# Kernel optimization log

Measured on AMD Instinct MI355X. Metric: run time of the kernel, lower is better.

The kernel has to match this reference:

```python
import jax, jax.numpy as jnp
import numpy as np

CUTOFF = 5.0
P = 6               # envelope polynomial power
NUM_RBF = 6
NUM_SBF = 7
EMBED = 128
TYPE_EMBED = 64
OUT_EMBED = 256
INT_EMBED = 64      # angle_int_embed_size
BASIS_EMBED = 8
N_BLOCKS = 4
N_DENSE_OUT = 3
N_RES_BEFORE = 1
N_RES_AFTER = 2
N_SPECIES = 16
NUM_TARGETS = 1
N_ATOMS = 4096
N_EDGES = 65536
N_TRIPLETS = 524288

# first 6 positive roots of spherical Bessel j_l, l = 0..6
BESSEL_ZEROS = np.array([
    [3.141593, 6.283185, 9.424778, 12.566371, 15.707963, 18.849556],
    [4.493409, 7.725252, 10.904122, 14.066194, 17.220755, 20.371303],
    [5.763459, 9.095011, 12.322941, 15.514603, 18.689036, 21.853874],
    [6.987932, 10.417119, 13.698023, 16.923621, 20.121806, 23.304247],
    [8.182561, 11.704907, 15.039665, 18.301256, 21.525418, 24.727566],
    [9.355812, 12.966530, 16.354710, 19.653152, 22.904551, 26.126750],
    [10.512835, 14.207392, 17.647975, 20.983463, 24.262768, 27.507868]], dtype=np.float32)

act = jax.nn.silu  # swish


def envelope(x):
    a = -(P + 1) * (P + 2) / 2.0
    b = float(P * (P + 2))
    c = -P * (P + 1) / 2.0
    env = 1.0 / x + a * x ** (P - 1) + b * x ** P + c * x ** (P + 1)
    return jnp.where(x < 1.0, env, 0.0)


def radial_bessel(d):
    # d: (E,) -> (E, NUM_RBF)
    x = d / CUTOFF
    n = jnp.arange(1, NUM_RBF + 1, dtype=jnp.float32)
    return np.float32(np.sqrt(2.0 / CUTOFF)) * envelope(x)[:, None] * jnp.sin(jnp.pi * n[None, :] * x[:, None])


def spherical_basis(d_kj, angles, triplet_mask):
    # d_kj: (T,), angles: (T,) -> (T, NUM_SBF * NUM_RBF)
    x = jnp.maximum(d_kj / CUTOFF, 1e-6)
    env = envelope(x)
    zeros = jnp.asarray(BESSEL_ZEROS)
    radial = []
    for l in range(NUM_SBF):
        a = zeros[l][None, :] * x[:, None]           # (T, NUM_RBF)
        j0 = jnp.sin(a) / a
        if l == 0:
            radial.append(j0)
            continue
        j1 = jnp.sin(a) / a ** 2 - jnp.cos(a) / a
        jm2, jm1 = j0, j1
        for ll in range(2, l + 1):
            jm2, jm1 = jm1, (2 * ll - 1) / a * jm1 - jm2
        radial.append(jm1)
    radial = jnp.stack(radial, axis=1)               # (T, NUM_SBF, NUM_RBF)
    ct = jnp.cos(angles)
    Pl = [jnp.ones_like(ct), ct]
    for l in range(2, NUM_SBF):
        Pl.append(((2 * l - 1) * ct * Pl[l - 1] - (l - 1) * Pl[l - 2]) / l)
    sph = jnp.stack([np.float32(np.sqrt((2 * l + 1) / (4.0 * np.pi))) * Pl[l] for l in range(NUM_SBF)], axis=1)  # (T, NUM_SBF)
    sbf = (env[:, None, None] * radial * sph[:, :, None]).reshape(-1, NUM_SBF * NUM_RBF)
    return jnp.where(triplet_mask[:, None], sbf, 0.0)


def _forward(distances, angles, species_embed, emb_rbf_w, emb_rbf_b, emb_dense_w, emb_dense_b,
             out_rbf_w, out_up_w, out_dense_w, out_dense_b, out_final_w,
             int_ji_w, int_ji_b, int_kj_w, int_kj_b, int_rbf1_w, int_rbf2_w, int_down_w,
             int_sbf1_w, int_sbf2_w, int_up_w, int_res1_w, int_res1_b, int_skip_w, int_skip_b,
             int_res2_w, int_res2_b,
             species, idx_i, idx_j, reduce_to_ji, expand_to_kj, edge_mask, triplet_mask):
    n_particles = species.shape[0]
    n_edges = distances.shape[0]
    d = jnp.where(edge_mask, distances, 2.0 * CUTOFF)       # masked edges -> env = 0
    rbf = radial_bessel(d)                                  # (E, 6)
    sbf = spherical_basis(d[expand_to_kj], angles, triplet_mask)  # (T, 42)

    # embedding block
    h = species_embed[species]                              # (N, 64)
    rbf_emb = rbf @ emb_rbf_w + emb_rbf_b                   # (E, 128)
    m = act(jnp.concatenate([h[idx_j], h[idx_i], rbf_emb], axis=-1) @ emb_dense_w + emb_dense_b)

    def output_block(i, msg):
        atom = jax.ops.segment_sum((rbf @ out_rbf_w[i]) * msg, idx_i, num_segments=n_particles)
        atom = atom @ out_up_w[i]
        for k in range(N_DENSE_OUT):
            atom = act(atom @ out_dense_w[i, k] + out_dense_b[i, k])
        return atom @ out_final_w[i]

    out = output_block(0, m)
    for i in range(N_BLOCKS):
        x_ji = act(m @ int_ji_w[i] + int_ji_b[i])
        x_kj = act(m @ int_kj_w[i] + int_kj_b[i])
        x_kj = x_kj * ((rbf @ int_rbf1_w[i]) @ int_rbf2_w[i])
        x_kj = act(x_kj @ int_down_w[i])                    # (E, 64)
        x_kj = x_kj[expand_to_kj] * ((sbf @ int_sbf1_w[i]) @ int_sbf2_w[i])  # (T, 64)
        x_kj = jax.ops.segment_sum(x_kj, reduce_to_ji, num_segments=n_edges)
        x_kj = act(x_kj @ int_up_w[i])
        hm = x_ji + x_kj
        for r in range(N_RES_BEFORE):
            hm = hm + act(act(hm @ int_res1_w[i, r, 0] + int_res1_b[i, r, 0]) @ int_res1_w[i, r, 1] + int_res1_b[i, r, 1])
        m = act(hm @ int_skip_w[i] + int_skip_b[i]) + m
        for r in range(N_RES_AFTER):
            m = m + act(act(m @ int_res2_w[i, r, 0] + int_res2_b[i, r, 0]) @ int_res2_w[i, r, 1] + int_res2_b[i, r, 1])
        out = out + output_block(i + 1, m)
    return out


def setup_inputs() -> dict:
    key = jax.random.key(0)
    ks = iter(jax.random.split(key, 40))
    def nrm(shape, fan_in):
        return jax.random.normal(next(ks), shape, dtype=jnp.float32) / np.float32(np.sqrt(fan_in))
    inp = {}
    inp['distances'] = 0.5 + 4.45 * jax.random.uniform(next(ks), (N_EDGES,), dtype=jnp.float32)
    inp['angles'] = jnp.pi * jax.random.uniform(next(ks), (N_TRIPLETS,), dtype=jnp.float32)
    inp['species_embed'] = jax.random.normal(next(ks), (N_SPECIES, TYPE_EMBED), dtype=jnp.float32)
    inp['emb_rbf_w'] = nrm((NUM_RBF, EMBED), NUM_RBF)
    inp['emb_rbf_b'] = jnp.zeros((EMBED,), jnp.float32)
    inp['emb_dense_w'] = nrm((2 * TYPE_EMBED + EMBED, EMBED), 2 * TYPE_EMBED + EMBED)
    inp['emb_dense_b'] = jnp.zeros((EMBED,), jnp.float32)
    nb1 = N_BLOCKS + 1
    inp['out_rbf_w'] = nrm((nb1, NUM_RBF, EMBED), NUM_RBF)
    inp['out_up_w'] = nrm((nb1, EMBED, OUT_EMBED), EMBED)
    inp['out_dense_w'] = nrm((nb1, N_DENSE_OUT, OUT_EMBED, OUT_EMBED), OUT_EMBED)
    inp['out_dense_b'] = jnp.zeros((nb1, N_DENSE_OUT, OUT_EMBED), jnp.float32)
    inp['out_final_w'] = nrm((nb1, OUT_EMBED, NUM_TARGETS), OUT_EMBED)
    inp['int_ji_w'] = nrm((N_BLOCKS, EMBED, EMBED), EMBED)
    inp['int_ji_b'] = jnp.zeros((N_BLOCKS, EMBED), jnp.float32)
    inp['int_kj_w'] = nrm((N_BLOCKS, EMBED, EMBED), EMBED)
    inp['int_kj_b'] = jnp.zeros((N_BLOCKS, EMBED), jnp.float32)
    inp['int_rbf1_w'] = nrm((N_BLOCKS, NUM_RBF, BASIS_EMBED), NUM_RBF)
    inp['int_rbf2_w'] = nrm((N_BLOCKS, BASIS_EMBED, EMBED), BASIS_EMBED)
    inp['int_down_w'] = nrm((N_BLOCKS, EMBED, INT_EMBED), EMBED)
    inp['int_sbf1_w'] = nrm((N_BLOCKS, NUM_SBF * NUM_RBF, BASIS_EMBED), NUM_SBF * NUM_RBF)
    inp['int_sbf2_w'] = nrm((N_BLOCKS, BASIS_EMBED, INT_EMBED), BASIS_EMBED)
    inp['int_up_w'] = nrm((N_BLOCKS, INT_EMBED, EMBED), INT_EMBED)
    inp['int_res1_w'] = nrm((N_BLOCKS, N_RES_BEFORE, 2, EMBED, EMBED), EMBED)
    inp['int_res1_b'] = jnp.zeros((N_BLOCKS, N_RES_BEFORE, 2, EMBED), jnp.float32)
    inp['int_skip_w'] = nrm((N_BLOCKS, EMBED, EMBED), EMBED)
    inp['int_skip_b'] = jnp.zeros((N_BLOCKS, EMBED), jnp.float32)
    inp['int_res2_w'] = nrm((N_BLOCKS, N_RES_AFTER, 2, EMBED, EMBED), EMBED)
    inp['int_res2_b'] = jnp.zeros((N_BLOCKS, N_RES_AFTER, 2, EMBED), jnp.float32)
    inp['species'] = jax.random.randint(next(ks), (N_ATOMS,), 0, N_SPECIES)
    inp['idx_i'] = jax.random.randint(next(ks), (N_EDGES,), 0, N_ATOMS)
    inp['idx_j'] = jax.random.randint(next(ks), (N_EDGES,), 0, N_ATOMS)
    inp['reduce_to_ji'] = jax.random.randint(next(ks), (N_TRIPLETS,), 0, N_EDGES)
    inp['expand_to_kj'] = jax.random.randint(next(ks), (N_TRIPLETS,), 0, N_EDGES)
    inp['edge_mask'] = jnp.ones((N_EDGES,), dtype=bool)
    inp['triplet_mask'] = jnp.ones((N_TRIPLETS,), dtype=bool)
    return inp


def reference(distances, angles, species_embed, emb_rbf_w, emb_rbf_b, emb_dense_w, emb_dense_b,
              out_rbf_w, out_up_w, out_dense_w, out_dense_b, out_final_w,
              int_ji_w, int_ji_b, int_kj_w, int_kj_b, int_rbf1_w, int_rbf2_w, int_down_w,
              int_sbf1_w, int_sbf2_w, int_up_w, int_res1_w, int_res1_b, int_skip_w, int_skip_b,
              int_res2_w, int_res2_b,
              species, idx_i, idx_j, reduce_to_ji, expand_to_kj, edge_mask, triplet_mask):
    return _forward(distances, angles, species_embed, emb_rbf_w, emb_rbf_b, emb_dense_w, emb_dense_b,
                    out_rbf_w, out_up_w, out_dense_w, out_dense_b, out_final_w,
                    int_ji_w, int_ji_b, int_kj_w, int_kj_b, int_rbf1_w, int_rbf2_w, int_down_w,
                    int_sbf1_w, int_sbf2_w, int_up_w, int_res1_w, int_res1_b, int_skip_w, int_skip_b,
                    int_res2_w, int_res2_b,
                    species, idx_i, idx_j, reduce_to_ji, expand_to_kj, edge_mask, triplet_mask)
```

## Files before the change

### kernel.cpp

```cpp
#include <hip/hip_runtime.h>
#include <cmath>

typedef __attribute__((ext_vector_type(8))) short bfrag;
typedef __attribute__((ext_vector_type(4))) float f32x4;

__device__ __forceinline__ float silu_f(float x) {
    return x * __builtin_amdgcn_rcpf(1.0f + __expf(-x));
}
__device__ __forceinline__ unsigned short f2bf(float f) {
    unsigned u = __float_as_uint(f);
    unsigned r = (u + 0x7fff + ((u >> 16) & 1)) >> 16;
    return (unsigned short)r;
}
__device__ __forceinline__ float bf2f(unsigned short h) {
    return __uint_as_float(((unsigned)h) << 16);
}
__device__ __forceinline__ unsigned packbf2(float lo, float hi) {
    return ((unsigned)f2bf(hi) << 16) | (unsigned)f2bf(lo);
}
__device__ __forceinline__ unsigned cvtpk2(float a, float b) {
    unsigned r;
    asm("v_cvt_pk_bf16_f32 %0, %1, %2" : "=v"(r) : "v"(a), "v"(b));
    return r;
}
__device__ __forceinline__ uint2 pk4(float a, float b, float c, float d) {
    return make_uint2(cvtpk2(a, b), cvtpk2(c, d));
}

template <int KSTEPS, int S, int NS, int ST>
__device__ __forceinline__ void mfma_stage_T(
    const unsigned short* Xs,
    const unsigned short* __restrict__ Whi, const unsigned short* __restrict__ Wlo,
    int Kdim, int arow0, int bcol0, int r16, int kg, f32x4 (&acc)[S][NS]) {
    #pragma unroll
    for (int s = 0; s < S; s++)
        #pragma unroll
        for (int ns = 0; ns < NS; ns++) acc[s][ns] = (f32x4)0.f;
    #pragma unroll
    for (int ks = 0; ks < KSTEPS; ks++) {
        int k0 = ks * 32;
        bfrag wh[NS], wl[NS];
        #pragma unroll
        for (int ns = 0; ns < NS; ns++) {
            size_t o = (size_t)(bcol0 + ns * 16 + r16) * Kdim + k0 + kg * 8;
            wh[ns] = *(const bfrag*)&Whi[o];
            wl[ns] = *(const bfrag*)&Wlo[o];
        }
        #pragma unroll
        for (int s = 0; s < S; s++) {
            bfrag xh = *(const bfrag*)&Xs[(arow0 + s * 16 + r16) * ST + k0 + kg * 8];
            #pragma unroll
            for (int ns = 0; ns < NS; ns++) {
                acc[s][ns] = __builtin_amdgcn_mfma_f32_16x16x32_bf16(wh[ns], xh, acc[s][ns], 0, 0, 0);
                acc[s][ns] = __builtin_amdgcn_mfma_f32_16x16x32_bf16(wl[ns], xh, acc[s][ns], 0, 0, 0);
            }
        }
    }
}

__global__ __launch_bounds__(256) void rbf_kernel(const float* __restrict__ d,
                                                  float* __restrict__ rbf, int E) {
    int e = blockIdx.x * 256 + threadIdx.x;
    if (e >= E) return;
    float x = d[e] * 0.2f;
    float env = 0.0f;
    if (x < 1.0f) {
        float x2 = x * x;
        float x5 = x2 * x2 * x;
        env = 1.0f / x + x5 * (-28.0f + x * (48.0f - 21.0f * x));
    }
    const float SQ = 0.63245553f;
    float px = 3.14159265358979f * x;
    #pragma unroll
    for (int n = 1; n <= 6; n++) {
        rbf[e * 6 + n - 1] = SQ * env * __sinf(px * (float)n);
    }
}

__global__ __launch_bounds__(128) void embed_pre_kernel(
    const float* __restrict__ se, const float* __restrict__ erw,
    const float* __restrict__ erb, const float* __restrict__ edw,
    float* __restrict__ HWj, float* __restrict__ HWi,
    float* __restrict__ W3, float* __restrict__ b3) {
    int c = threadIdx.x;
    for (int s = 0; s < 16; s++) {
        float aj = 0.f, ai = 0.f;
        for (int k = 0; k < 64; k++) {
            float h = se[s * 64 + k];
            aj += h * edw[k * 128 + c];
            ai += h * edw[(64 + k) * 128 + c];
        }
        HWj[s * 128 + c] = aj;
        HWi[s * 128 + c] = ai;
    }
    for (int r = 0; r < 6; r++) {
        float a = 0.f;
        for (int k = 0; k < 128; k++) a += erw[r * 128 + k] * edw[(128 + k) * 128 + c];
        W3[r * 128 + c] = a;
    }
    float a = 0.f;
    for (int k = 0; k < 128; k++) a += erb[k] * edw[(128 + k) * 128 + c];
    b3[c] = a;
}

__global__ __launch_bounds__(256) void embed_kernel(
    const float* __restrict__ rbf, const int* __restrict__ species,
    const int* __restrict__ idx_i, const int* __restrict__ idx_j,
    const float* __restrict__ HWj, const float* __restrict__ HWi,
    const float* __restrict__ W3, const float* __restrict__ b3,
    const float* __restrict__ edb, float* __restrict__ m) {
    int gid = blockIdx.x * 256 + threadIdx.x;
    int e = gid >> 7, c = gid & 127;
    int sj = species[idx_j[e]];
    int si = species[idx_i[e]];
    float v = HWj[sj * 128 + c] + HWi[si * 128 + c] + b3[c] + edb[c];
    #pragma unroll
    for (int k = 0; k < 6; k++) v += rbf[e * 6 + k] * W3[k * 128 + c];
    m[gid] = silu_f(v);
}

__global__ __launch_bounds__(256) void wconv_kernel(
    const float* __restrict__ W, unsigned short* __restrict__ hi,
    unsigned short* __restrict__ lo, int K, int N) {
    __shared__ float t[32][33];
    int b = blockIdx.z;
    int n0 = blockIdx.x * 32, k0 = blockIdx.y * 32;
    const float* Wb = W + (size_t)b * K * N;
    int tid = threadIdx.x;
    int r = tid >> 3, cg = tid & 7;
    float4 v = *(const float4*)&Wb[(size_t)(k0 + r) * N + n0 + cg * 4];
    t[r][cg * 4 + 0] = v.x;
    t[r][cg * 4 + 1] = v.y;
    t[r][cg * 4 + 2] = v.z;
    t[r][cg * 4 + 3] = v.w;
    __syncthreads();
    int nl = tid >> 3, kg = tid & 7;
    short4 h4, l4;
// ... 39 lines not shown
        bfrag wh[2], wl[2];
        #pragma unroll
        for (int ns = 0; ns < 2; ns++) {
            size_t o = (size_t)(bn + bcol0 + ns * 16 + r16) * K + k0 + kg * 8;
            wh[ns] = *(const bfrag*)&Whi[o];
            wl[ns] = *(const bfrag*)&Wlo[o];
        }
        #pragma unroll
        for (int s = 0; s < 2; s++) {
            bfrag xh = *(const bfrag*)&Xs[(arow0 + s * 16 + r16) * 40 + kg * 8];
            #pragma unroll
            for (int ns = 0; ns < 2; ns++) {
                acc[s][ns] = __builtin_amdgcn_mfma_f32_16x16x32_bf16(wh[ns], xh, acc[s][ns], 0, 0, 0);
                acc[s][ns] = __builtin_amdgcn_mfma_f32_16x16x32_bf16(wl[ns], xh, acc[s][ns], 0, 0, 0);
            }
        }
        __syncthreads();
    }
    #pragma unroll
    for (int s = 0; s < 2; s++) {
        int mm = bm + arow0 + s * 16 + r16;
        #pragma unroll
        for (int ns = 0; ns < 2; ns++) {
            int n0 = bn + bcol0 + ns * 16 + kg * 4;
            float bv[4] = {0.f, 0.f, 0.f, 0.f};
            if (BIAS) {
                float4 b4 = *(const float4*)&bias[n0];
                bv[0] = b4.x; bv[1] = b4.y; bv[2] = b4.z; bv[3] = b4.w;
            }
            float4 o;
            float* op = (float*)&o;
            #pragma unroll
            for (int r = 0; r < 4; r++) {
                float v = acc[s][ns][r] + bv[r];
                if (ACT) v = silu_f(v);
                op[r] = v;
            }
            if (RES) {
                float4 rv = *(const float4*)&resid[(size_t)mm * N + n0];
                o.x += rv.x; o.y += rv.y; o.z += rv.z; o.w += rv.w;
            }
            *(float4*)&Y[(size_t)mm * N + n0] = o;
        }
    }
}

__global__ __launch_bounds__(512, 4) void outchain_kernel(
    const float* __restrict__ atom2,
    const unsigned short* __restrict__ odh, const unsigned short* __restrict__ odl,
    const float* __restrict__ odb, const float* __restrict__ wf,
    float* __restrict__ out) {
    __shared__ unsigned short Xs[64 * 264];
    __shared__ float rsum[64];
    int tid = threadIdx.x, bm = blockIdx.x * 64;
    int wid = tid >> 6, lane = tid & 63;
    int wr = wid >> 2, wc = wid & 3;
    int r16 = lane & 15, kg = lane >> 4;
    int arow0 = wr * 32, bcol0 = wc * 64;
    if (tid < 64) rsum[tid] = 0.f;

    #pragma unroll
    for (int p = 0; p < 8; p++) {
        int idx = tid + p * 512, row = idx >> 6, cg = idx & 63;
        float4 v = *(const float4*)&atom2[(size_t)(bm + row) * 256 + cg * 4];
        *(uint2*)&Xs[row * 264 + cg * 4] = pk4(v.x, v.y, v.z, v.w);
    }
    __syncthreads();

    f32x4 acc[2][4];
    #pragma unroll
    for (int st = 0; st < 3; st++) {
        mfma_stage_T<8, 2, 4, 264>(Xs, odh + (size_t)st * 65536, odl + (size_t)st * 65536,
                                   256, arow0, bcol0, r16, kg, acc);
        const float* bb = odb + st * 256;
        __syncthreads();
        if (st < 2) {
            #pragma unroll
            for (int s = 0; s < 2; s++)
                #pragma unroll
                for (int ns = 0; ns < 4; ns++) {
                    int n0 = bcol0 + ns * 16 + kg * 4;
                    float4 b4 = *(const float4*)&bb[n0];
                    *(uint2*)&Xs[(arow0 + s * 16 + r16) * 264 + n0] =
                        pk4(silu_f(acc[s][0 + ns][0] + b4.x), silu_f(acc[s][ns][1] + b4.y),
                            silu_f(acc[s][ns][2] + b4.z), silu_f(acc[s][ns][3] + b4.w));
                }
            __syncthreads();
        } else {
            #pragma unroll
            for (int s = 0; s < 2; s++) {
                float part = 0.f;
                #pragma unroll
                for (int ns = 0; ns < 4; ns++) {
                    int n0 = bcol0 + ns * 16 + kg * 4;
                    float4 b4 = *(const float4*)&bb[n0];
                    float4 w4 = *(const float4*)&wf[n0];
                    part += silu_f(acc[s][ns][0] + b4.x) * w4.x;
                    part += silu_f(acc[s][ns][1] + b4.y) * w4.y;
                    part += silu_f(acc[s][ns][2] + b4.z) * w4.z;
                    part += silu_f(acc[s][ns][3] + b4.w) * w4.w;
                }
                atomicAdd(&rsum[arow0 + s * 16 + r16], part);
            }
        }
    }
    __syncthreads();
    if (tid < 64) out[bm + tid] += rsum[tid];
}

__global__ __launch_bounds__(512, 4) void downpath_kernel(
    const float* __restrict__ m, const float* __restrict__ rbf,
    const float* __restrict__ rbf1, const float* __restrict__ rbf2,
    const unsigned short* __restrict__ jih, const unsigned short* __restrict__ jil,
    const float* __restrict__ jib,
    const unsigned short* __restrict__ kjh, const unsigned short* __restrict__ kjl,
    const float* __restrict__ kjb,
    const unsigned short* __restrict__ dnh, const unsigned short* __restrict__ dnl,
    float* __restrict__ xji, float* __restrict__ xdown) {
    __shared__ unsigned short Xs[64 * 136];
    __shared__ float G8t[8][64];
    __shared__ float Rs[8][128];
    int tid = threadIdx.x, bm = blockIdx.x * 64;
    int wid = tid >> 6, lane = tid & 63;
    int wr = wid >> 2, wc = wid & 3;
    int r16 = lane & 15, kg = lane >> 4;
    int arow0 = wr * 32, bcol0 = wc * 32;

    #pragma unroll
    for (int p = 0; p < 4; p++) {
        int idx = tid + p * 512, row = idx >> 5, cg = idx & 31;
        float4 v = *(const float4*)&m[(size_t)(bm + row) * 128 + cg * 4];
        *(uint2*)&Xs[row * 136 + cg * 4] = pk4(v.x, v.y, v.z, v.w);
    }
    if (tid < 64) {
        float rv[6];
        #pragma unroll
        for (int k = 0; k < 6; k++) rv[k] = rbf[(size_t)(bm + tid) * 6 + k];
        #pragma unroll
        for (int p = 0; p < 8; p++) {
            float a = 0.f;
            #pragma unroll
            for (int k = 0; k < 6; k++) a += rv[k] * rbf1[k * 8 + p];
            G8t[p][tid] = a;
        }
    }
    for (int i = tid; i < 1024; i += 512) Rs[i >> 7][i & 127] = rbf2[i];
    __syncthreads();

    f32x4 acc[2][2];
    mfma_stage_T<4, 2, 2, 136>(Xs, jih, jil, 128, arow0, bcol0, r16, kg, acc);
    #pragma unroll
    for (int s = 0; s < 2; s++) {
        int mm = bm + arow0 + s * 16 + r16;
        #pragma unroll
        for (int ns = 0; ns < 2; ns++) {
            int n0 = bcol0 + ns * 16 + kg * 4;
            float4 b4 = *(const float4*)&jib[n0];
            float4 o;
            o.x = silu_f(acc[s][ns][0] + b4.x);
            o.y = silu_f(acc[s][ns][1] + b4.y);
            o.z = silu_f(acc[s][ns][2] + b4.z);
            o.w = silu_f(acc[s][ns][3] + b4.w);
            *(float4*)&xji[(size_t)mm * 128 + n0] = o;
        }
    }
    mfma_stage_T<4, 2, 2, 136>(Xs, kjh, kjl, 128, arow0, bcol0, r16, kg, acc);
    f32x4 val[2][2];
    #pragma unroll
    for (int s = 0; s < 2; s++) {
        int mrow = arow0 + s * 16 + r16;
        float g8v[8];
        #pragma unroll
        for (int p = 0; p < 8; p++) g8v[p] = G8t[p][mrow];
        #pragma unroll
        for (int ns = 0; ns < 2; ns++) {
            int n0 = bcol0 + ns * 16 + kg * 4;
            float4 b4 = *(const float4*)&kjb[n0];
            float bb[4] = {b4.x, b4.y, b4.z, b4.w};
            #pragma unroll
            for (int r = 0; r < 4; r++) {
                float g = 0.f;
                #pragma unroll
                for (int p = 0; p < 8; p++) g = fmaf(g8v[p], Rs[p][n0 + r], g);
                val[s][ns][r] = silu_f(acc[s][ns][r] + bb[r]) * g;
            }
        }
    }
    __syncthreads();
    #pragma unroll
    for (int s = 0; s < 2; s++)
        #pragma unroll
        for (int ns = 0; ns < 2; ns++)
            *(uint2*)&Xs[(arow0 + s * 16 + r16) * 136 + bcol0 + ns * 16 + kg * 4] =
                pk4(val[s][ns][0], val[s][ns][1], val[s][ns][2], val[s][ns][3]);
    __syncthreads();
    {
        int ar2 = (wid >> 1) * 16, wc2 = wid & 1;
        f32x4 a2[1][2];
        mfma_stage_T<4, 1, 2, 136>(Xs, dnh, dnl, 128, ar2, wc2 * 32, r16, kg, a2);
        int mm = bm + ar2 + r16;
        #pragma unroll
        for (int ns = 0; ns < 2; ns++) {
            int n0 = wc2 * 32 + ns * 16 + kg * 4;
            float4 o;
            o.x = silu_f(a2[0][ns][0]);
            o.y = silu_f(a2[0][ns][1]);
            o.z = silu_f(a2[0][ns][2]);
            o.w = silu_f(a2[0][ns][3]);
            *(float4*)&xdown[(size_t)mm * 64 + n0] = o;
        }
    }
}

__global__ __launch_bounds__(512, 4) void chain_kernel(
    const float* __restrict__ seg, const float* __restrict__ xji, float* __restrict__ m,
    const unsigned short* __restrict__ uph, const unsigned short* __restrict__ upl,
    const unsigned short* __restrict__ r1h, const unsigned short* __restrict__ r1l,
    const float* __restrict__ r1b,
    const unsigned short* __restrict__ skh, const unsigned short* __restrict__ skl,
    const float* __restrict__ skb,
    const unsigned short* __restrict__ r2h, const unsigned short* __restrict__ r2l,
    const float* __restrict__ r2b) {
    __shared__ unsigned short Xs[64 * 136];
    int tid = threadIdx.x, bm = blockIdx.x * 64;
    int wid = tid >> 6, lane = tid & 63;
    int wr = wid >> 2, wc = wid & 3;
    int r16 = lane & 15, kg = lane >> 4;
    int arow0 = wr * 32, bcol0 = wc * 32;

    #pragma unroll
    for (int p = 0; p < 2; p++) {
        int idx = tid + p * 512, row = idx >> 4, cg = idx & 15;
        float4 v = *(const float4*)&seg[(size_t)(bm + row) * 64 + cg * 4];
        *(uint2*)&Xs[row * 136 + cg * 4] = pk4(v.x, v.y, v.z, v.w);
    }
    __syncthreads();

    f32x4 acc[2][2], res[2][2];

    mfma_stage_T<2, 2, 2, 136>(Xs, uph, upl, 64, arow0, bcol0, r16, kg, acc);
    #pragma unroll
    for (int s = 0; s < 2; s++) {
        int mm = bm + arow0 + s * 16 + r16;
        #pragma unroll
        for (int ns = 0; ns < 2; ns++) {
            int n0 = bcol0 + ns * 16 + kg * 4;
            float4 xv = *(const float4*)&xji[(size_t)mm * 128 + n0];
            res[s][ns][0] = silu_f(acc[s][ns][0]) + xv.x;
            res[s][ns][1] = silu_f(acc[s][ns][1]) + xv.y;
            res[s][ns][2] = silu_f(acc[s][ns][2]) + xv.z;
            res[s][ns][3] = silu_f(acc[s][ns][3]) + xv.w;
        }
    }
    __syncthreads();
    #pragma unroll
    for (int s = 0; s < 2; s++)
        #pragma unroll
        for (int ns = 0; ns < 2; ns++)
            *(uint2*)&Xs[(arow0 + s * 16 + r16) * 136 + bcol0 + ns * 16 + kg * 4] =
                pk4(res[s][ns][0], res[s][ns][1], res[s][ns][2], res[s][ns][3]);
    __syncthreads();

    mfma_stage_T<4, 2, 2, 136>(Xs, r1h, r1l, 128, arow0, bcol0, r16, kg, acc);
    __syncthreads();
    #pragma unroll
    for (int s = 0; s < 2; s++)
        #pragma unroll
        for (int ns = 0; ns < 2; ns++) {
            int n0 = bcol0 + ns * 16 + kg * 4;
            float4 b4 = *(const float4*)&r1b[n0];
            *(uint2*)&Xs[(arow0 + s * 16 + r16) * 136 + n0] =
                pk4(silu_f(acc[s][ns][0] + b4.x), silu_f(acc[s][ns][1] + b4.y),
                    silu_f(acc[s][ns][2] + b4.z), silu_f(acc[s][ns][3] + b4.w));
        }
    __syncthreads();
    mfma_stage_T<4, 2, 2, 136>(Xs, r1h + 16384, r1l + 16384, 128, arow0, bcol0, r16, kg, acc);
    #pragma unroll
    for (int s = 0; s < 2; s++)
        #pragma unroll
        for (int ns = 0; ns < 2; ns++) {
            int n0 = bcol0 + ns * 16 + kg * 4;
            float4 b4 = *(const float4*)&r1b[128 + n0];
            res[s][ns][0] += silu_f(acc[s][ns][0] + b4.x);
            res[s][ns][1] += silu_f(acc[s][ns][1] + b4.y);
            res[s][ns][2] += silu_f(acc[s][ns][2] + b4.z);
            res[s][ns][3] += silu_f(acc[s][ns][3] + b4.w);
        }
    __syncthreads();
    #pragma unroll
    for (int s = 0; s < 2; s++)
        #pragma unroll
        for (int ns = 0; ns < 2; ns++)
            *(uint2*)&Xs[(arow0 + s * 16 + r16) * 136 + bcol0 + ns * 16 + kg * 4] =
                pk4(res[s][ns][0], res[s][ns][1], res[s][ns][2], res[s][ns][3]);
    __syncthreads();

    mfma_stage_T<4, 2, 2, 136>(Xs, skh, skl, 128, arow0, bcol0, r16, kg, acc);
    #pragma unroll
    for (int s = 0; s < 2; s++) {
        int mm = bm + arow0 + s * 16 + r16;
        #pragma unroll
        for (int ns = 0; ns < 2; ns++) {
            int n0 = bcol0 + ns * 16 + kg * 4;
            float4 b4 = *(const float4*)&skb[n0];
            float4 mv = *(const float4*)&m[(size_t)mm * 128 + n0];
            res[s][ns][0] = silu_f(acc[s][ns][0] + b4.x) + mv.x;
            res[s][ns][1] = silu_f(acc[s][ns][1] + b4.y) + mv.y;
            res[s][ns][2] = silu_f(acc[s][ns][2] + b4.z) + mv.z;
            res[s][ns][3] = silu_f(acc[s][ns][3] + b4.w) + mv.w;
        }
    }
    __syncthreads();
    #pragma unroll
    for (int s = 0; s < 2; s++)
        #pragma unroll
        for (int ns = 0; ns < 2; ns++)
            *(uint2*)&Xs[(arow0 + s * 16 + r16) * 136 + bcol0 + ns * 16 + kg * 4] =
                pk4(res[s][ns][0], res[s][ns][1], res[s][ns][2], res[s][ns][3]);
    __syncthreads();

    #pragma unroll
    for (int rr = 0; rr < 2; rr++) {
        const unsigned short* wh = r2h + (size_t)rr * 2 * 16384;
        const unsigned short* wl = r2l + (size_t)rr * 2 * 16384;
        const float* bb = r2b + (size_t)rr * 2 * 128;
        mfma_stage_T<4, 2, 2, 136>(Xs, wh, wl, 128, arow0, bcol0, r16, kg, acc);
        __syncthreads();
        #pragma unroll
        for (int s = 0; s < 2; s++)
            #pragma unroll
            for (int ns = 0; ns < 2; ns++) {
                int n0 = bcol0 + ns * 16 + kg * 4;
                float4 b4 = *(const float4*)&bb[n0];
                *(uint2*)&Xs[(arow0 + s * 16 + r16) * 136 + n0] =
                    pk4(silu_f(acc[s][ns][0] + b4.x), silu_f(acc[s][ns][1] + b4.y),
                        silu_f(acc[s][ns][2] + b4.z), silu_f(acc[s][ns][3] + b4.w));
            }
        __syncthreads();
        mfma_stage_T<4, 2, 2, 136>(Xs, wh + 16384, wl + 16384, 128, arow0, bcol0, r16, kg, acc);
        #pragma unroll
        for (int s = 0; s < 2; s++)
            #pragma unroll
            for (int ns = 0; ns < 2; ns++) {
                int n0 = bcol0 + ns * 16 + kg * 4;
                float4 b4 = *(const float4*)&bb[128 + n0];
                res[s][ns][0] += silu_f(acc[s][ns][0] + b4.x);
                res[s][ns][1] += silu_f(acc[s][ns][1] + b4.y);
                res[s][ns][2] += silu_f(acc[s][ns][2] + b4.z);
                res[s][ns][3] += silu_f(acc[s][ns][3] + b4.w);
            }
        if (rr == 0) {
            __syncthreads();
            #pragma unroll
            for (int s = 0; s < 2; s++)
                #pragma unroll
                for (int ns = 0; ns < 2; ns++)
                    *(uint2*)&Xs[(arow0 + s * 16 + r16) * 136 + bcol0 + ns * 16 + kg * 4] =
                        pk4(res[s][ns][0], res[s][ns][1], res[s][ns][2], res[s][ns][3]);
            __syncthreads();
        }
    }
    #pragma unroll
    for (int s = 0; s < 2; s++) {
        int mm = bm + arow0 + s * 16 + r16;
        #pragma unroll
        for (int ns = 0; ns < 2; ns++) {
            int n0 = bcol0 + ns * 16 + kg * 4;
            float4 o;
            o.x = res[s][ns][0]; o.y = res[s][ns][1];
            o.z = res[s][ns][2]; o.w = res[s][ns][3];
            *(float4*)&m[(size_t)mm * 128 + n0] = o;
        }
    }
}

__global__ __launch_bounds__(256) void outseg_kernel(
    const float* __restrict__ rbf, const float* __restrict__ orw,
    const float* __restrict__ m, const int* __restrict__ idx_i,
    float* __restrict__ atom) {
    int gid = blockIdx.x * 256 + threadIdx.x;
    int e = gid >> 7, c = gid & 127;
    float s = 0.f;
    #pragma unroll
    for (int k = 0; k < 6; k++) s += rbf[e * 6 + k] * orw[k * 128 + c];
    atomicAdd(&atom[(size_t)idx_i[e] * 128 + c], s * m[gid]);
}

__global__ __launch_bounds__(256) void hist_kernel(const int* __restrict__ rji,
                                                   int* __restrict__ hist) {
    int t = blockIdx.x * 256 + threadIdx.x;
    atomicAdd(&hist[rji[t]], 1);
}

__global__ __launch_bounds__(256) void scan1_kernel(const int* __restrict__ hist,
                                                    int* __restrict__ bsum) {
    __shared__ int s[256];
    int i = threadIdx.x;
    s[i] = hist[blockIdx.x * 256 + i];
    __syncthreads();
    for (int o = 128; o; o >>= 1) {
        if (i < o) s[i] += s[i + o];
        __syncthreads();
    }
    if (!i) bsum[blockIdx.x] = s[0];
}

__global__ __launch_bounds__(256) void scan2_kernel(const int* __restrict__ bsum,
                                                    int* __restrict__ boff) {
    __shared__ int s[256];
    int i = threadIdx.x;
    int own = bsum[i];
    s[i] = own;
    __syncthreads();
    for (int o = 1; o < 256; o <<= 1) {
        int v = (i >= o) ? s[i - o] : 0;
        __syncthreads();
        s[i] += v;
        __syncthreads();
    }
    boff[i] = s[i] - own;
}

__global__ __launch_bounds__(256) void scan3_kernel(const int* __restrict__ hist,
                                                    const int* __restrict__ boff,
                                                    int* __restrict__ rows,
                                                    int* __restrict__ cursor, int T) {
    __shared__ int s[256];
    int i = threadIdx.x, b = blockIdx.x;
    int h = hist[b * 256 + i];
    s[i] = h;
    __syncthreads();
    for (int o = 1; o < 256; o <<= 1) {
        int v = (i >= o) ? s[i - o] : 0;
        __syncthreads();
        s[i] += v;
        __syncthreads();
    }
    int excl = s[i] - h + boff[b];
    rows[b * 256 + i] = excl;
    cursor[b * 256 + i] = excl;
    if (b == gridDim.x - 1 && i == 255) rows[b * 256 + 256] = T;
}

__global__ __launch_bounds__(256) void scatter_kernel(
    const int* __restrict__ rji, const int* __restrict__ ekj,
    int* __restrict__ cursor, int* __restrict__ perm, int* __restrict__ ekjs) {
// ... 165 lines not shown
    float* HWj = ws + off;   off += 16 * 128;
    float* HWi = ws + off;   off += 16 * 128;
    float* W3  = ws + off;   off += 6 * 128;
    float* b3  = ws + off;   off += 128;
    float* atom1 = ws + off; off += (size_t)NA * 128;
    float* atom2 = ws + off; off += (size_t)NA * 256;
    float* atom3 = ws + off; off += (size_t)NA * 256;
    float* seg = B;

    unsigned short* wb = (unsigned short*)(ws + off);
    size_t wo = 0;
    unsigned short* ji_h = wb + wo;  wo += 4 * 16384;
    unsigned short* ji_l = wb + wo;  wo += 4 * 16384;
    unsigned short* kj_h = wb + wo;  wo += 4 * 16384;
    unsigned short* kj_l = wb + wo;  wo += 4 * 16384;
    unsigned short* dn_h = wb + wo;  wo += 4 * 8192;
    unsigned short* dn_l = wb + wo;  wo += 4 * 8192;
    unsigned short* up_h = wb + wo;  wo += 4 * 8192;
    unsigned short* up_l = wb + wo;  wo += 4 * 8192;
    unsigned short* r1_h = wb + wo;  wo += 8 * 16384;
    unsigned short* r1_l = wb + wo;  wo += 8 * 16384;
    unsigned short* sk_h = wb + wo;  wo += 4 * 16384;
    unsigned short* sk_l = wb + wo;  wo += 4 * 16384;
    unsigned short* r2_h = wb + wo;  wo += 16 * 16384;
    unsigned short* r2_l = wb + wo;  wo += 16 * 16384;
    unsigned short* ou_h = wb + wo;  wo += 5 * 32768;
    unsigned short* ou_l = wb + wo;  wo += 5 * 32768;
    unsigned short* od_h = wb + wo;  wo += 15 * 65536;
    unsigned short* od_l = wb + wo;  wo += 15 * 65536;
    unsigned short* t32 = wb + wo;   wo += (size_t)4 * T * 8;
    int* ip    = (int*)(wb + wo);
    size_t io  = 0;
    int* hist   = ip + io;  io += E;
    int* rows   = ip + io;  io += E + 64;
    int* cursor = ip + io;  io += E;
    int* bsum   = ip + io;  io += 256;
    int* boff   = ip + io;  io += 256;
    int* perm   = ip + io;  io += T;
    int* ekjs   = ip + io;  io += T;

    float* out = (float*)d_out;
    hipMemsetAsync(out, 0, (size_t)out_size * sizeof(float), stream);

    hipMemsetAsync(hist, 0, (size_t)E * sizeof(int), stream);
    hist_kernel<<<T / 256, 256, 0, stream>>>(reduce_ji, hist);
    scan1_kernel<<<E / 256, 256, 0, stream>>>(hist, bsum);
    scan2_kernel<<<1, 256, 0, stream>>>(bsum, boff);
    scan3_kernel<<<E / 256, 256, 0, stream>>>(hist, boff, rows, cursor, T);
    scatter_kernel<<<T / 256, 256, 0, stream>>>(reduce_ji, expand_kj, cursor, perm, ekjs);
    sbf_pre_kernel<<<T / 256, 256, 0, stream>>>(distances, angles, perm, ekjs,
                                                int_sbf1_w, t32, T);

    wconv_kernel<<<dim3(4, 4, 4), 256, 0, stream>>>(int_ji_w, ji_h, ji_l, 128, 128);
    wconv_kernel<<<dim3(4, 4, 4), 256, 0, stream>>>(int_kj_w, kj_h, kj_l, 128, 128);
    wconv_kernel<<<dim3(2, 4, 4), 256, 0, stream>>>(int_down_w, dn_h, dn_l, 128, 64);
    wconv_kernel<<<dim3(4, 2, 4), 256, 0, stream>>>(int_up_w, up_h, up_l, 64, 128);
    wconv_kernel<<<dim3(4, 4, 8), 256, 0, stream>>>(int_res1_w, r1_h, r1_l, 128, 128);
    wconv_kernel<<<dim3(4, 4, 4), 256, 0, stream>>>(int_skip_w, sk_h, sk_l, 128, 128);
    wconv_kernel<<<dim3(4, 4, 16), 256, 0, stream>>>(int_res2_w, r2_h, r2_l, 128, 128);
    wconv_kernel<<<dim3(8, 4, 5), 256, 0, stream>>>(out_up_w, ou_h, ou_l, 128, 256);
    wconv_kernel<<<dim3(8, 8, 15), 256, 0, stream>>>(out_dense_w, od_h, od_l, 256, 256);

    rbf_kernel<<<E / 256, 256, 0, stream>>>(distances, rbf, E);
    embed_pre_kernel<<<1, 128, 0, stream>>>(species_emb, emb_rbf_w, emb_rbf_b,
                                            emb_dense_w, HWj, HWi, W3, b3);
    embed_kernel<<<E * 128 / 256, 256, 0, stream>>>(rbf, species, idx_i, idx_j,
                                                    HWj, HWi, W3, b3, emb_dense_b, m);

    auto outblock = [&](int i, const float* msg) {
        hipMemsetAsync(atom1, 0, (size_t)NA * 128 * sizeof(float), stream);
        outseg_kernel<<<E * 128 / 256, 256, 0, stream>>>(
            rbf, out_rbf_w + (size_t)i * 6 * 128, msg, idx_i, atom1);
        mfma_gemmT<0, 0, 0><<<dim3(NA / 64, 2), 512, 0, stream>>>(
            atom1, ou_h + (size_t)i * 32768, ou_l + (size_t)i * 32768,
            nullptr, nullptr, atom2, NA, 128, 256);
        outchain_kernel<<<NA / 64, 512, 0, stream>>>(
            atom2, od_h + (size_t)i * 3 * 65536, od_l + (size_t)i * 3 * 65536,
            out_dense_b + (size_t)i * 3 * 256, out_final_w + (size_t)i * 256, out);
    };

    outblock(0, m);

    for (int i = 0; i < 4; i++) {
        downpath_kernel<<<E / 64, 512, 0, stream>>>(
            m, rbf, int_rbf1_w + (size_t)i * 48, int_rbf2_w + (size_t)i * 1024,
            ji_h + (size_t)i * 16384, ji_l + (size_t)i * 16384, int_ji_b + (size_t)i * 128,
            kj_h + (size_t)i * 16384, kj_l + (size_t)i * 16384, int_kj_b + (size_t)i * 128,
            dn_h + (size_t)i * 8192, dn_l + (size_t)i * 8192,
            A, D);
        seg_gather_kernel<<<E * 64 / 256, 256, 0, stream>>>(
            t32 + (size_t)i * T * 8, ekjs, rows, D,
            int_sbf2_w + (size_t)i * 8 * 64, seg, E);
        chain_kernel<<<E / 64, 512, 0, stream>>>(
            seg, A, m,
            up_h + (size_t)i * 8192, up_l + (size_t)i * 8192,
            r1_h + (size_t)i * 32768, r1_l + (size_t)i * 32768, int_res1_b + (size_t)i * 256,
            sk_h + (size_t)i * 16384, sk_l + (size_t)i * 16384, int_skip_b + (size_t)i * 128,
            r2_h + (size_t)i * 65536, r2_l + (size_t)i * 65536, int_res2_b + (size_t)i * 512);
        outblock(i + 1, m);
    }
}
```

Baseline: 1.742 ms.

## Enlarge row tiles, double-buffer LDS and prefetch weights in chain kernels

Doubles the row tile of the downpath and chain kernels from 64 to 128 edges, so each warp computes four 16-row subtiles and every loaded weight fragment is reused across more rows. Adds ping-pong LDS buffers (XsA/XsB), which removes the barrier that had to come before each activation write-back. Adds a new MFMA stage that prefetches the next K-step of weights into registers. In exchange the kernels use more registers and about 70KB of LDS per block, which lowers occupancy and halves the grid size.

```diff
diff --git a/kernel.cpp b/kernel.cpp
--- a/kernel.cpp
+++ b/kernel.cpp
@@ -53,6 +53,45 @@
             for (int ns = 0; ns < NS; ns++) {
                 acc[s][ns] = __builtin_amdgcn_mfma_f32_16x16x32_bf16(wh[ns], xh, acc[s][ns], 0, 0, 0);
                 acc[s][ns] = __builtin_amdgcn_mfma_f32_16x16x32_bf16(wl[ns], xh, acc[s][ns], 0, 0, 0);
+            }
+        }
+    }
+}
+
+template <int KSTEPS, int S, int NS, int ST>
+__device__ __forceinline__ void mfma_stage_pp(
+    const unsigned short* Xs,
+    const unsigned short* __restrict__ Whi, const unsigned short* __restrict__ Wlo,
+    int Kdim, int arow0, int bcol0, int r16, int kg, f32x4 (&acc)[S][NS]) {
+    bfrag wh[2][NS], wl[2][NS];
+    #pragma unroll
+    for (int ns = 0; ns < NS; ns++) {
+        size_t o = (size_t)(bcol0 + ns * 16 + r16) * Kdim + kg * 8;
+        wh[0][ns] = *(const bfrag*)&Whi[o];
+        wl[0][ns] = *(const bfrag*)&Wlo[o];
+    }
+    #pragma unroll
+    for (int s = 0; s < S; s++)
+        #pragma unroll
+        for (int ns = 0; ns < NS; ns++) acc[s][ns] = (f32x4)0.f;
+    #pragma unroll
+    for (int ks = 0; ks < KSTEPS; ks++) {
+        const int cur = ks & 1, nxt = cur ^ 1;
+        if (ks + 1 < KSTEPS) {
+            #pragma unroll
+            for (int ns = 0; ns < NS; ns++) {
+                size_t o = (size_t)(bcol0 + ns * 16 + r16) * Kdim + (ks + 1) * 32 + kg * 8;
+                wh[nxt][ns] = *(const bfrag*)&Whi[o];
+                wl[nxt][ns] = *(const bfrag*)&Wlo[o];
+            }
+        }
+        #pragma unroll
+        for (int s = 0; s < S; s++) {
+            bfrag xh = *(const bfrag*)&Xs[(arow0 + s * 16 + r16) * ST + ks * 32 + kg * 8];
+            #pragma unroll
+            for (int ns = 0; ns < NS; ns++) {
+                acc[s][ns] = __builtin_amdgcn_mfma_f32_16x16x32_bf16(wh[cur][ns], xh, acc[s][ns], 0, 0, 0);
+                acc[s][ns] = __builtin_amdgcn_mfma_f32_16x16x32_bf16(wl[cur][ns], xh, acc[s][ns], 0, 0, 0);
             }
         }
     }
@@ -258,7 +297,7 @@
                     int n0 = bcol0 + ns * 16 + kg * 4;
                     float4 b4 = *(const float4*)&bb[n0];
                     *(uint2*)&Xs[(arow0 + s * 16 + r16) * 264 + n0] =
-                        pk4(silu_f(acc[s][0 + ns][0] + b4.x), silu_f(acc[s][ns][1] + b4.y),
+                        pk4(silu_f(acc[s][ns][0] + b4.x), silu_f(acc[s][ns][1] + b4.y),
                             silu_f(acc[s][ns][2] + b4.z), silu_f(acc[s][ns][3] + b4.w));
                 }
             __syncthreads();
@@ -293,22 +332,23 @@
     const float* __restrict__ kjb,
     const unsigned short* __restrict__ dnh, const unsigned short* __restrict__ dnl,
     float* __restrict__ xji, float* __restrict__ xdown) {
-    __shared__ unsigned short Xs[64 * 136];
-    __shared__ float G8t[8][64];
+    __shared__ unsigned short XsA[128 * 136];
+    __shared__ unsigned short XsB[128 * 136];
+    __shared__ float G8t[8][128];
     __shared__ float Rs[8][128];
-    int tid = threadIdx.x, bm = blockIdx.x * 64;
+    int tid = threadIdx.x, bm = blockIdx.x * 128;
     int wid = tid >> 6, lane = tid & 63;
     int wr = wid >> 2, wc = wid & 3;
     int r16 = lane & 15, kg = lane >> 4;
-    int arow0 = wr * 32, bcol0 = wc * 32;
-
-    #pragma unroll
-    for (int p = 0; p < 4; p++) {
+    int arow0 = wr * 64, bcol0 = wc * 32;
+
+    #pragma unroll
+    for (int p = 0; p < 8; p++) {
         int idx = tid + p * 512, row = idx >> 5, cg = idx & 31;
         float4 v = *(const float4*)&m[(size_t)(bm + row) * 128 + cg * 4];
-        *(uint2*)&Xs[row * 136 + cg * 4] = pk4(v.x, v.y, v.z, v.w);
-    }
-    if (tid < 64) {
+        *(uint2*)&XsA[row * 136 + cg * 4] = pk4(v.x, v.y, v.z, v.w);
+    }
+    if (tid < 128) {
         float rv[6];
         #pragma unroll
         for (int k = 0; k < 6; k++) rv[k] = rbf[(size_t)(bm + tid) * 6 + k];
@@ -323,10 +363,10 @@
     for (int i = tid; i < 1024; i += 512) Rs[i >> 7][i & 127] = rbf2[i];
     __syncthreads();
 
-    f32x4 acc[2][2];
-    mfma_stage_T<4, 2, 2, 136>(Xs, jih, jil, 128, arow0, bcol0, r16, kg, acc);
-    #pragma unroll
-    for (int s = 0; s < 2; s++) {
+    f32x4 acc[4][2];
+    mfma_stage_pp<4, 4, 2, 136>(XsA, jih, jil, 128, arow0, bcol0, r16, kg, acc);
+    #pragma unroll
+    for (int s = 0; s < 4; s++) {
         int mm = bm + arow0 + s * 16 + r16;
         #pragma unroll
         for (int ns = 0; ns < 2; ns++) {
@@ -340,10 +380,9 @@
             *(float4*)&xji[(size_t)mm * 128 + n0] = o;
         }
     }
-    mfma_stage_T<4, 2, 2, 136>(Xs, kjh, kjl, 128, arow0, bcol0, r16, kg, acc);
-    f32x4 val[2][2];
-    #pragma unroll
-    for (int s = 0; s < 2; s++) {
+    mfma_stage_pp<4, 4, 2, 136>(XsA, kjh, kjl, 128, arow0, bcol0, r16, kg, acc);
+    #pragma unroll
+    for (int s = 0; s < 4; s++) {
         int mrow = arow0 + s * 16 + r16;
         float g8v[8];
         #pragma unroll
@@ -353,37 +392,36 @@
             int n0 = bcol0 + ns * 16 + kg * 4;
             float4 b4 = *(const float4*)&kjb[n0];
             float bb[4] = {b4.x, b4.y, b4.z, b4.w};
+            float v[4];
             #pragma unroll
             for (int r = 0; r < 4; r++) {
                 float g = 0.f;
                 #pragma unroll
                 for (int p = 0; p < 8; p++) g = fmaf(g8v[p], Rs[p][n0 + r], g);
-                val[s][ns][r] = silu_f(acc[s][ns][r] + bb[r]) * g;
-            }
-        }
-    }
-    __syncthreads();
-    #pragma unroll
-    for (int s = 0; s < 2; s++)
-        #pragma unroll
-        for (int ns = 0; ns < 2; ns++)
-            *(uint2*)&Xs[(arow0 + s * 16 + r16) * 136 + bcol0 + ns * 16 + kg * 4] =
-                pk4(val[s][ns][0], val[s][ns][1], val[s][ns][2], val[s][ns][3]);
+                v[r] = silu_f(acc[s][ns][r] + bb[r]) * g;
+            }
+            *(uint2*)&XsB[mrow * 136 + n0] = pk4(v[0], v[1], v[2], v[3]);
+        }
+    }
     __syncthreads();
     {
-        int ar2 = (wid >> 1) * 16, wc2 = wid & 1;
-        f32x4 a2[1][2];
-        mfma_stage_T<4, 1, 2, 136>(Xs, dnh, dnl, 128, ar2, wc2 * 32, r16, kg, a2);
-        int mm = bm + ar2 + r16;
-        #pragma unroll
-        for (int ns = 0; ns < 2; ns++) {
-            int n0 = wc2 * 32 + ns * 16 + kg * 4;
-            float4 o;
-            o.x = silu_f(a2[0][ns][0]);
-            o.y = silu_f(a2[0][ns][1]);
-            o.z = silu_f(a2[0][ns][2]);
-            o.w = silu_f(a2[0][ns][3]);
-            *(float4*)&xdown[(size_t)mm * 64 + n0] = o;
+        int wr2 = wid >> 1, wc2 = wid & 1;
+        int ar2 = wr2 * 32, bc2 = wc2 * 32;
+        f32x4 a2[2][2];
+        mfma_stage_pp<4, 2, 2, 136>(XsB, dnh, dnl, 128, ar2, bc2, r16, kg, a2);
+        #pragma unroll
+        for (int s = 0; s < 2; s++) {
+            int mm = bm + ar2 + s * 16 + r16;
+            #pragma unroll
+            for (int ns = 0; ns < 2; ns++) {
+                int n0 = bc2 + ns * 16 + kg * 4;
+                float4 o;
+                o.x = silu_f(a2[s][ns][0]);
+                o.y = silu_f(a2[s][ns][1]);
+                o.z = silu_f(a2[s][ns][2]);
+                o.w = silu_f(a2[s][ns][3]);
+                *(float4*)&xdown[(size_t)mm * 64 + n0] = o;
+            }
         }
     }
 }
@@ -397,26 +435,61 @@
     const float* __restrict__ skb,
     const unsigned short* __restrict__ r2h, const unsigned short* __restrict__ r2l,
     const float* __restrict__ r2b) {
-    __shared__ unsigned short Xs[64 * 136];
-    int tid = threadIdx.x, bm = blockIdx.x * 64;
+    __shared__ unsigned short XsA[128 * 136];
+    __shared__ unsigned short XsB[128 * 136];
+    int tid = threadIdx.x, bm = blockIdx.x * 128;
     int wid = tid >> 6, lane = tid & 63;
     int wr = wid >> 2, wc = wid & 3;
     int r16 = lane & 15, kg = lane >> 4;
-    int arow0 = wr * 32, bcol0 = wc * 32;
-
-    #pragma unroll
-    for (int p = 0; p < 2; p++) {
+    int arow0 = wr * 64, bcol0 = wc * 32;
+
+    #pragma unroll
+    for (int p = 0; p < 4; p++) {
         int idx = tid + p * 512, row = idx >> 4, cg = idx & 15;
         float4 v = *(const float4*)&seg[(size_t)(bm + row) * 64 + cg * 4];
-        *(uint2*)&Xs[row * 136 + cg * 4] = pk4(v.x, v.y, v.z, v.w);
-    }
-    __syncthreads();
-
-    f32x4 acc[2][2], res[2][2];
-
-    mfma_stage_T<2, 2, 2, 136>(Xs, uph, upl, 64, arow0, bcol0, r16, kg, acc);
-    #pragma unroll
-    for (int s = 0; s < 2; s++) {
+        *(uint2*)&XsA[row * 136 + cg * 4] = pk4(v.x, v.y, v.z, v.w);
+    }
+    __syncthreads();
+
+    f32x4 acc[4][2], res[4][2];
+
+    auto store_frags = [&](unsigned short* Xd, const f32x4 (&v)[4][2]) {
+        #pragma unroll
+        for (int s = 0; s < 4; s++)
+            #pragma unroll
+            for (int ns = 0; ns < 2; ns++)
+                *(uint2*)&Xd[(arow0 + s * 16 + r16) * 136 + bcol0 + ns * 16 + kg * 4] =
+                    pk4(v[s][ns][0], v[s][ns][1], v[s][ns][2], v[s][ns][3]);
+    };
+    auto store_act = [&](unsigned short* Xd, const f32x4 (&a)[4][2], const float* bb) {
+        #pragma unroll
+        for (int s = 0; s < 4; s++)
+            #pragma unroll
+            for (int ns = 0; ns < 2; ns++) {
+                int n0 = bcol0 + ns * 16 + kg * 4;
+                float4 b4 = *(const float4*)&bb[n0];
+                *(uint2*)&Xd[(arow0 + s * 16 + r16) * 136 + n0] =
+                    pk4(silu_f(a[s][ns][0] + b4.x), silu_f(a[s][ns][1] + b4.y),
+                        silu_f(a[s][ns][2] + b4.z), silu_f(a[s][ns][3] + b4.w));
+            }
+    };
+    auto accum_res = [&](const f32x4 (&a)[4][2], const float* bb) {
+        #pragma unroll
+        for (int s = 0; s < 4; s++)
+            #pragma unroll
+            for (int ns = 0; ns < 2; ns++) {
+                int n0 = bcol0 + ns * 16 + kg * 4;
+                float4 b4 = *(const float4*)&bb[n0];
+                res[s][ns][0] += silu_f(a[s][ns][0] + b4.x);
+                res[s][ns][1] += silu_f(a[s][ns][1] + b4.y);
+                res[s][ns][2] += silu_f(a[s][ns][2] + b4.z);
+                res[s][ns][3] += silu_f(a[s][ns][3] + b4.w);
+            }
+    };
+
+    mfma_stage_pp<2, 4, 2, 136>(XsA, uph, upl, 64, arow0, bcol0, r16, kg, acc);
+    #pragma unroll
+    for (int s = 0; s < 4; s++) {
         int mm = bm + arow0 + s * 16 + r16;
         #pragma unroll
         for (int ns = 0; ns < 2; ns++) {
@@ -428,52 +501,20 @@
             res[s][ns][3] = silu_f(acc[s][ns][3]) + xv.w;
         }
     }
-    __syncthreads();
-    #pragma unroll
-    for (int s = 0; s < 2; s++)
-        #pragma unroll
-        for (int ns = 0; ns < 2; ns++)
-            *(uint2*)&Xs[(arow0 + s * 16 + r16) * 136 + bcol0 + ns * 16 + kg * 4] =
-                pk4(res[s][ns][0], res[s][ns][1], res[s][ns][2], res[s][ns][3]);
-    __syncthreads();
-
-    mfma_stage_T<4, 2, 2, 136>(Xs, r1h, r1l, 128, arow0, bcol0, r16, kg, acc);
-    __syncthreads();
-    #pragma unroll
-    for (int s = 0; s < 2; s++)
-        #pragma unroll
-        for (int ns = 0; ns < 2; ns++) {
-            int n0 = bcol0 + ns * 16 + kg * 4;
-            float4 b4 = *(const float4*)&r1b[n0];
-            *(uint2*)&Xs[(arow0 + s * 16 + r16) * 136 + n0] =
-                pk4(silu_f(acc[s][ns][0] + b4.x), silu_f(acc[s][ns][1] + b4.y),
-                    silu_f(acc[s][ns][2] + b4.z), silu_f(acc[s][ns][3] + b4.w));
-        }
-    __syncthreads();
-    mfma_stage_T<4, 2, 2, 136>(Xs, r1h + 16384, r1l + 16384, 128, arow0, bcol0, r16, kg, acc);
-    #pragma unroll
-    for (int s = 0; s < 2; s++)
-        #pragma unroll
-        for (int ns = 0; ns < 2; ns++) {
-            int n0 = bcol0 + ns * 16 + kg * 4;
-            float4 b4 = *(const float4*)&r1b[128 + n0];
-            res[s][ns][0] += silu_f(acc[s][ns][0] + b4.x);
-            res[s][ns][1] += silu_f(acc[s][ns][1] + b4.y);
-            res[s][ns][2] += silu_f(acc[s][ns][2] + b4.z);
-            res[s][ns][3] += silu_f(acc[s][ns][3] + b4.w);
-        }
-    __syncthreads();
-    #pragma unroll
-    for (int s = 0; s < 2; s++)
-        #pragma unroll
-        for (int ns = 0; ns < 2; ns++)
-            *(uint2*)&Xs[(arow0 + s * 16 + r16) * 136 + bcol0 + ns * 16 + kg * 4] =
-                pk4(res[s][ns][0], res[s][ns][1], res[s][ns][2], res[s][ns][3]);
-    __syncthreads();
-
-    mfma_stage_T<4, 2, 2, 136>(Xs, skh, skl, 128, arow0, bcol0, r16, kg, acc);
-    #pragma unroll
-    for (int s = 0; s < 2; s++) {
+    store_frags(XsB, res);
+    __syncthreads();
+
+    mfma_stage_pp<4, 4, 2, 136>(XsB, r1h, r1l, 128, arow0, bcol0, r16, kg, acc);
+    store_act(XsA, acc, r1b);
+    __syncthreads();
+    mfma_stage_pp<4, 4, 2, 136>(XsA, r1h + 16384, r1l + 16384, 128, arow0, bcol0, r16, kg, acc);
+    accum_res(acc, r1b + 128);
+    store_frags(XsB, res);
+    __syncthreads();
+
+    mfma_stage_pp<4, 4, 2, 136>(XsB, skh, skl, 128, arow0, bcol0, r16, kg, acc);
+    #pragma unroll
+    for (int s = 0; s < 4; s++) {
         int mm = bm + arow0 + s * 16 + r16;
         #pragma unroll
         for (int ns = 0; ns < 2; ns++) {
@@ -486,58 +527,23 @@
             res[s][ns][3] = silu_f(acc[s][ns][3] + b4.w) + mv.w;
         }
     }
-    __syncthreads();
-    #pragma unroll
-    for (int s = 0; s < 2; s++)
-        #pragma unroll
-        for (int ns = 0; ns < 2; ns++)
-            *(uint2*)&Xs[(arow0 + s * 16 + r16) * 136 + bcol0 + ns * 16 + kg * 4] =
-                pk4(res[s][ns][0], res[s][ns][1], res[s][ns][2], res[s][ns][3]);
-    __syncthreads();
-
-    #pragma unroll
-    for (int rr = 0; rr < 2; rr++) {
-        const unsigned short* wh = r2h + (size_t)rr * 2 * 16384;
-        const unsigned short* wl = r2l + (size_t)rr * 2 * 16384;
-        const float* bb = r2b + (size_t)rr * 2 * 128;
-        mfma_stage_T<4, 2, 2, 136>(Xs, wh, wl, 128, arow0, bcol0, r16, kg, acc);
-        __syncthreads();
-        #pragma unroll
-        for (int s = 0; s < 2; s++)
-            #pragma unroll
-            for (int ns = 0; ns < 2; ns++) {
-                int n0 = bcol0 + ns * 16 + kg * 4;
-                float4 b4 = *(const float4*)&bb[n0];
-                *(uint2*)&Xs[(arow0 + s * 16 + r16) * 136 + n0] =
-                    pk4(silu_f(acc[s][ns][0] + b4.x), silu_f(acc[s][ns][1] + b4.y),
-                        silu_f(acc[s][ns][2] + b4.z), silu_f(acc[s][ns][3] + b4.w));
-            }
-        __syncthreads();
-        mfma_stage_T<4, 2, 2, 136>(Xs, wh + 16384, wl + 16384, 128, arow0, bcol0, r16, kg, acc);
-        #pragma unroll
-        for (int s = 0; s < 2; s++)
-            #pragma unroll
-            for (int ns = 0; ns < 2; ns++) {
-                int n0 = bcol0 + ns * 16 + kg * 4;
-                float4 b4 = *(const float4*)&bb[128 + n0];
-                res[s][ns][0] += silu_f(acc[s][ns][0] + b4.x);
-                res[s][ns][1] += silu_f(acc[s][ns][1] + b4.y);
-                res[s][ns][2] += silu_f(acc[s][ns][2] + b4.z);
-                res[s][ns][3] += silu_f(acc[s][ns][3] + b4.w);
-            }
-        if (rr == 0) {
-            __syncthreads();
-            #pragma unroll
-            for (int s = 0; s < 2; s++)
-                #pragma unroll
-                for (int ns = 0; ns < 2; ns++)
-                    *(uint2*)&Xs[(arow0 + s * 16 + r16) * 136 + bcol0 + ns * 16 + kg * 4] =
-                        pk4(res[s][ns][0], res[s][ns][1], res[s][ns][2], res[s][ns][3]);
-            __syncthreads();
-        }
-    }
-    #pragma unroll
-    for (int s = 0; s < 2; s++) {
+    store_frags(XsA, res);
+    __syncthreads();
+
+    mfma_stage_pp<4, 4, 2, 136>(XsA, r2h, r2l, 128, arow0, bcol0, r16, kg, acc);
+    store_act(XsB, acc, r2b);
+    __syncthreads();
+    mfma_stage_pp<4, 4, 2, 136>(XsB, r2h + 16384, r2l + 16384, 128, arow0, bcol0, r16, kg, acc);
+    accum_res(acc, r2b + 128);
+    store_frags(XsA, res);
+    __syncthreads();
+    mfma_stage_pp<4, 4, 2, 136>(XsA, r2h + 32768, r2l + 32768, 128, arow0, bcol0, r16, kg, acc);
+    store_act(XsB, acc, r2b + 256);
+    __syncthreads();
+    mfma_stage_pp<4, 4, 2, 136>(XsB, r2h + 49152, r2l + 49152, 128, arow0, bcol0, r16, kg, acc);
+    accum_res(acc, r2b + 384);
+    #pragma unroll
+    for (int s = 0; s < 4; s++) {
         int mm = bm + arow0 + s * 16 + r16;
         #pragma unroll
         for (int ns = 0; ns < 2; ns++) {
@@ -869,7 +875,7 @@
     outblock(0, m);
 
     for (int i = 0; i < 4; i++) {
-        downpath_kernel<<<E / 64, 512, 0, stream>>>(
+        downpath_kernel<<<E / 128, 512, 0, stream>>>(
             m, rbf, int_rbf1_w + (size_t)i * 48, int_rbf2_w + (size_t)i * 1024,
             ji_h + (size_t)i * 16384, ji_l + (size_t)i * 16384, int_ji_b + (size_t)i * 128,
             kj_h + (size_t)i * 16384, kj_l + (size_t)i * 16384, int_kj_b + (size_t)i * 128,
@@ -878,7 +884,7 @@
         seg_gather_kernel<<<E * 64 / 256, 256, 0, stream>>>(
             t32 + (size_t)i * T * 8, ekjs, rows, D,
             int_sbf2_w + (size_t)i * 8 * 64, seg, E);
-        chain_kernel<<<E / 64, 512, 0, stream>>>(
+        chain_kernel<<<E / 128, 512, 0, stream>>>(
             seg, A, m,
             up_h + (size_t)i * 8192, up_l + (size_t)i * 8192,
             r1_h + (size_t)i * 32768, r1_l + (size_t)i * 32768, int_res1_b + (size_t)i * 256,
```

After: 1.497 ms. -14.0%, faster.
